# Optimization experiments

Measured on AMD Instinct MI355X. Metric: run time of the kernel, lower is better.

Reference implementation:

```python
import math
import jax, jax.numpy as jnp
import numpy as np

B, S, D, H = 4, 2048, 1024, 16
DK = D // H


def setup_inputs() -> dict:
    key = jax.random.key(0)
    kx, kq, kk, kv, ko = jax.random.split(key, 5)
    scale = 1.0 / math.sqrt(D)
    return {
        "x": jax.random.normal(kx, (B, S, D), dtype=jnp.float32),
        "wq": jax.random.normal(kq, (D, D), dtype=jnp.float32) * scale,
        "wk": jax.random.normal(kk, (D, D), dtype=jnp.float32) * scale,
        "wv": jax.random.normal(kv, (D, D), dtype=jnp.float32) * scale,
        "wo": jax.random.normal(ko, (D, D), dtype=jnp.float32) * scale,
    }


def reference(x, wq, wk, wv, wo):
    b, s, d = x.shape
    # projections -> [b, h, s, dk]
    def split_heads(t):
        return t.reshape(b, s, H, DK).transpose(0, 2, 1, 3)
    q = split_heads(x @ wq)
    k = split_heads(x @ wk)
    v = split_heads(x @ wv)
    # scores [b, h, s, s], scaled by sqrt(d_k)
    scores = jnp.einsum('bhqd,bhkd->bhqk', q, k) / math.sqrt(DK)
    causal = jnp.tril(jnp.ones((s, s), dtype=bool))  # [s, s]
    scores = jnp.where(causal[None, None, :, :], scores, -jnp.inf)
    weights = jax.nn.softmax(scores, axis=-1)
    weights = jnp.nan_to_num(weights, nan=0.0)
    attn = jnp.einsum('bhqk,bhkd->bhqd', weights, v)
    attn = attn.transpose(0, 2, 1, 3).reshape(b, s, d)
    return attn @ wo
```

## Files before the change

### kernel.cpp

```cpp
#include <hip/hip_runtime.h>
#include <hip/hip_bf16.h>
#include <math.h>

#define B_ 4
#define S_ 2048
#define D_ 1024
#define H_ 16
#define DK_ 64

typedef __bf16 bf16;
typedef bf16 bf16x8 __attribute__((ext_vector_type(8)));
typedef float f32x4 __attribute__((ext_vector_type(4)));
typedef float f32x16 __attribute__((ext_vector_type(16)));

__device__ __forceinline__ int swz8(int row, int slot) {
    return row * 64 + ((slot ^ (row & 7)) << 3);
}
__device__ __forceinline__ unsigned packbf(float a, float b) {
    union { bf16 h[2]; unsigned u; } x;
    x.h[0] = (bf16)a; x.h[1] = (bf16)b;
    return x.u;
}
__device__ __forceinline__ void permswap(unsigned& x, unsigned& y) {
    asm("v_permlane32_swap_b32 %0, %1" : "+v"(x), "+v"(y));
}
__device__ __forceinline__ float fexp2(float x) {
#if __has_builtin(__builtin_amdgcn_exp2f)
    return __builtin_amdgcn_exp2f(x);
#else
    float r;
    asm("v_exp_f32 %0, %1" : "=v"(r) : "v"(x));
    return r;
#endif
}
__device__ __forceinline__ void gld16(bf16* lbase, const bf16* gsrc) {
    __builtin_amdgcn_global_load_lds(
        (const __attribute__((address_space(1))) unsigned*)gsrc,
        (__attribute__((address_space(3))) unsigned*)lbase, 16, 0, 0);
}

__global__ __launch_bounds__(256) void prep_kernel(const float* __restrict__ x,
                                                   const float* __restrict__ wq, const float* __restrict__ wk,
                                                   const float* __restrict__ wv, const float* __restrict__ wo,
                                                   bf16* __restrict__ xb, bf16* __restrict__ wqkvT,
                                                   bf16* __restrict__ woT) {
    __shared__ float t[32][33];
    const int bid = blockIdx.x;
    const int tid = threadIdx.x;
    if (bid < 4096) {
        const size_t i = ((size_t)bid * 256 + tid) * 8;
        const float4* src = (const float4*)(x + i);
        float4 f0 = src[0], f1 = src[1];
        bf16x8 v;
        v[0] = (bf16)f0.x; v[1] = (bf16)f0.y; v[2] = (bf16)f0.z; v[3] = (bf16)f0.w;
        v[4] = (bf16)f1.x; v[5] = (bf16)f1.y; v[6] = (bf16)f1.z; v[7] = (bf16)f1.w;
        *(bf16x8*)(xb + i) = v;
    } else {
        const int b2 = bid - 4096;
        const int z = b2 >> 10;
        const float* src = (z == 0) ? wq : (z == 1) ? wk : (z == 2) ? wv : wo;
        bf16* dst = (z < 3) ? (wqkvT + (size_t)z * 1024 * 1024) : woT;
        const int n0 = (b2 & 31) * 32, k0 = ((b2 >> 5) & 31) * 32;
        const int tx = tid & 31, ty = tid >> 5;
#pragma unroll
        for (int j = 0; j < 4; ++j)
            t[ty + j * 8][tx] = src[(size_t)(k0 + ty + j * 8) * 1024 + n0 + tx];
        __syncthreads();
#pragma unroll
        for (int j = 0; j < 4; ++j)
            dst[(size_t)(n0 + ty + j * 8) * 1024 + k0 + tx] = (bf16)t[tx][ty + j * 8];
    }
}

template <int MODE>
__global__ __launch_bounds__(256) void gemm_kernel(const bf16* __restrict__ A, const bf16* __restrict__ Bt,
                                                   void* o0, void* o1, void* o2,
                                                   int M, int N, int K, int NT) {
    __shared__ __align__(16) bf16 As[128 * 64];
    __shared__ __align__(16) bf16 Bs[128 * 64];
    const int tid = threadIdx.x;
    const int lane = tid & 63;
    const int w = tid >> 6;
    const int wm = w >> 1, wn = w & 1;
    const int g = lane >> 4, r16 = lane & 15;

    const int bid = blockIdx.x;
    const int qch = gridDim.x >> 3;
    const int wg = (bid & 7) * qch + (bid >> 3);
    const int mt = wg / NT, nt = wg % NT;
    const int m0 = mt * 128, n0 = nt * 128;

    const int srow = tid >> 3;
    const int sslot = (tid & 7) ^ (srow & 7);
    const bf16* ga = A + (size_t)(m0 + srow) * K + sslot * 8;
    const bf16* gb = Bt + (size_t)(n0 + srow) * K + sslot * 8;

    f32x4 acc[4][4] = {};

    for (int kt = 0; kt < K; kt += 64) {
#pragma unroll
        for (int p = 0; p < 4; ++p) {
            gld16(&As[p * 2048 + w * 512], ga + (size_t)p * 32 * K + kt);
            gld16(&Bs[p * 2048 + w * 512], gb + (size_t)p * 32 * K + kt);
        }
        __syncthreads();
#pragma unroll
        for (int k0 = 0; k0 < 2; ++k0) {
            bf16x8 af[4], bfr[4];
#pragma unroll
            for (int mf = 0; mf < 4; ++mf)
                af[mf] = *(const bf16x8*)&As[swz8(wm * 64 + mf * 16 + r16, 4 * k0 + g)];
#pragma unroll
            for (int nf = 0; nf < 4; ++nf)
                bfr[nf] = *(const bf16x8*)&Bs[swz8(wn * 64 + nf * 16 + r16, 4 * k0 + g)];
#pragma unroll
            for (int mf = 0; mf < 4; ++mf)
#pragma unroll
                for (int nf = 0; nf < 4; ++nf)
                    acc[mf][nf] = __builtin_amdgcn_mfma_f32_16x16x32_bf16(af[mf], bfr[nf], acc[mf][nf], 0, 0, 0);
        }
        __syncthreads();
    }

    if (MODE == 0) {
        const int seg = nt >> 3;
#pragma unroll
        for (int mf = 0; mf < 4; ++mf) {
#pragma unroll
            for (int nf = 0; nf < 4; ++nf) {
                const int col = n0 + wn * 64 + nf * 16 + r16;
                const int n1 = col & 1023;
                const int h = n1 >> 6, dk = n1 & 63;
                const int row0 = m0 + wm * 64 + mf * 16 + 4 * g;
                const int b = row0 >> 11, s0 = row0 & 2047;
                if (seg == 2) {
                    union { bf16 h4[4]; unsigned long long u; } pk;
#pragma unroll
                    for (int rr = 0; rr < 4; ++rr) pk.h4[rr] = (bf16)acc[mf][nf][rr];
                    *(unsigned long long*)((bf16*)o2 + (((size_t)b * H_ + h) * DK_ + dk) * S_ + s0) = pk.u;
                } else {
                    bf16* dst = (seg == 0) ? (bf16*)o0 : (bf16*)o1;
#pragma unroll
                    for (int rr = 0; rr < 4; ++rr)
                        dst[(((size_t)b * H_ + h) * S_ + s0 + rr) * DK_ + dk] = (bf16)acc[mf][nf][rr];
                }
            }
        }
    } else {
#pragma unroll
        for (int mf = 0; mf < 4; ++mf)
#pragma unroll
            for (int nf = 0; nf < 4; ++nf)
#pragma unroll
                for (int rr = 0; rr < 4; ++rr) {
                    int row = m0 + wm * 64 + mf * 16 + 4 * g + rr;
                    int col = n0 + wn * 64 + nf * 16 + r16;
                    ((float*)o0)[(size_t)row * N + col] = acc[mf][nf][rr];
                }
    }
}

__global__ __launch_bounds__(256, 4) void attn_kernel(const bf16* __restrict__ Q,
                                                      const bf16* __restrict__ Kb,
                                                      const bf16* __restrict__ Vt,
                                                      bf16* __restrict__ ctx) {
    __shared__ __align__(16) bf16 lds[4][4096];
    const int bh = blockIdx.x;
    const int qt = 15 - (int)blockIdx.y;
    const int tid = threadIdx.x;
    const int lane = tid & 63, w = tid >> 6;
    const int lq = lane & 31, hi = lane >> 5;
    const int q0 = qt * 128;
    const int q0w = q0 + w * 32;
    const int q = q0w + lq;
    const int njt = 2 * qt + 2;
    const float qscale = 0.125f * 1.44269504088896340736f;

    const int srow = tid >> 3;
    const int sslot = (tid & 7) ^ (srow & 7);
    const bf16* kg = Kb + ((size_t)bh * S_ + srow) * DK_ + sslot * 8;
    const bf16* vg = Vt + ((size_t)bh * DK_ + srow) * S_ + sslot * 8;

    bf16x8 qf[4];
    {
        const bf16* qp = Q + ((size_t)bh * S_ + q) * DK_ + hi * 8;
#pragma unroll
        for (int kc = 0; kc < 4; ++kc) {
            bf16x8 raw = *(const bf16x8*)(qp + kc * 16);
#pragma unroll
            for (int e = 0; e < 8; ++e) qf[kc][e] = (bf16)((float)raw[e] * qscale);
        }
    }

    f32x16 accd[2] = {};
    float lsum = 0.f;

    bf16x8 kreg0 = *(const bf16x8*)kg;
    bf16x8 kreg1 = *(const bf16x8*)(kg + 32 * DK_);
    bf16x8 vreg0 = *(const bf16x8*)vg;
    bf16x8 vreg1 = *(const bf16x8*)(vg + 32 * S_);

    for (int jt = 0; jt < njt; ++jt) {
        const int cur = jt & 1;
        *(bf16x8*)&lds[cur][tid * 8] = kreg0;
        *(bf16x8*)&lds[cur][tid * 8 + 2048] = kreg1;
        *(bf16x8*)&lds[2 + cur][tid * 8] = vreg0;
        *(bf16x8*)&lds[2 + cur][tid * 8 + 2048] = vreg1;
        if (jt + 1 < njt) {
            kreg0 = *(const bf16x8*)(kg + (size_t)(jt + 1) * 64 * DK_);
            kreg1 = *(const bf16x8*)(kg + (size_t)(jt + 1) * 64 * DK_ + 32 * DK_);
            vreg0 = *(const bf16x8*)(vg + (jt + 1) * 64);
            vreg1 = *(const bf16x8*)(vg + (jt + 1) * 64 + 32 * S_);
        }
        __syncthreads();

        if (jt * 64 <= q0w + 31) {
            f32x16 sacc[2];
#pragma unroll
            for (int c = 0; c < 2; ++c)
#pragma unroll
                for (int r = 0; r < 16; ++r) sacc[c][r] = -16.0f;
            __builtin_amdgcn_s_setprio(1);
#pragma unroll
            for (int kc = 0; kc < 4; ++kc) {
#pragma unroll
                for (int c = 0; c < 2; ++c) {
                    bf16x8 kf = *(const bf16x8*)&lds[cur][swz8(c * 32 + lq, kc * 2 + hi)];
                    sacc[c] = __builtin_amdgcn_mfma_f32_32x32x16_bf16(kf, qf[kc], sacc[c], 0, 0, 0);
                }
            }
            __builtin_amdgcn_s_setprio(0);

            if (jt * 64 + 63 > q0w) {
#pragma unroll
                for (int c = 0; c < 2; ++c)
#pragma unroll
                    for (int r = 0; r < 16; ++r) {
                        int key = jt * 64 + c * 32 + (r & 3) + 8 * (r >> 2) + 4 * hi;
                        if (key > q) sacc[c][r] = -INFINITY;
                    }
            }

#pragma unroll
            for (int c = 0; c < 2; ++c)
#pragma unroll
                for (int r = 0; r < 16; ++r) sacc[c][r] = fexp2(sacc[c][r]);

            float s8[8];
#pragma unroll
            for (int i = 0; i < 8; ++i)
                s8[i] = (sacc[0][i] + sacc[0][i + 8]) + (sacc[1][i] + sacc[1][i + 8]);
#pragma unroll
            for (int i = 0; i < 4; ++i) s8[i] += s8[i + 4];
            lsum += (s8[0] + s8[1]) + (s8[2] + s8[3]);

#pragma unroll
            for (int kc = 0; kc < 4; ++kc) {
                const int c = kc >> 1, kf2 = kc & 1;
                unsigned w0 = packbf(sacc[c][8 * kf2 + 0], sacc[c][8 * kf2 + 1]);
                unsigned w1 = packbf(sacc[c][8 * kf2 + 2], sacc[c][8 * kf2 + 3]);
                unsigned w2 = packbf(sacc[c][8 * kf2 + 4], sacc[c][8 * kf2 + 5]);
                unsigned w3 = packbf(sacc[c][8 * kf2 + 6], sacc[c][8 * kf2 + 7]);
                permswap(w0, w2);
                permswap(w1, w3);
                union { unsigned wd[4]; bf16x8 v; } u;
                u.wd[0] = w0; u.wd[1] = w1; u.wd[2] = w2; u.wd[3] = w3;
                __builtin_amdgcn_s_setprio(1);
#pragma unroll
                for (int dt = 0; dt < 2; ++dt) {
                    bf16x8 vf = *(const bf16x8*)&lds[2 + cur][swz8(dt * 32 + lq, kc * 2 + hi)];
                    accd[dt] = __builtin_amdgcn_mfma_f32_32x32x16_bf16(vf, u.v, accd[dt], 0, 0, 0);
                }
                __builtin_amdgcn_s_setprio(0);
            }
        }
    }

    __syncthreads();
    bf16* eb = &lds[0][0];
    const float rl = 1.0f / (lsum + __shfl_xor(lsum, 32));
    {
        const int rowb = (w * 32 + lq) * 128;
        const int rsw = (lq & 7) << 4;
#pragma unroll
        for (int dt = 0; dt < 2; ++dt)
#pragma unroll
            for (int rq = 0; rq < 4; ++rq) {
                union { bf16 h[4]; unsigned long long u64; } pk;
#pragma unroll
                for (int j = 0; j < 4; ++j) pk.h[j] = (bf16)(accd[dt][rq * 4 + j] * rl);
                int off = rowb + ((dt * 64 + rq * 16 + hi * 8) ^ rsw);
                *(unsigned long long*)((char*)eb + off) = pk.u64;
            }
    }
    __syncthreads();
    {
        const int row = tid >> 1, half = tid & 1;
        const int b = bh >> 4, h = bh & 15;
        bf16* op = ctx + ((size_t)b * S_ + q0 + row) * D_ + h * DK_ + half * 32;
#pragma unroll
        for (int i = 0; i < 4; ++i) {
            int sl = half * 4 + i;
            int sls = sl ^ (row & 7);
            bf16x8 v = *(const bf16x8*)((const char*)eb + row * 128 + sls * 16);
            *(bf16x8*)(op + i * 8) = v;
        }
    }
}

extern "C" void kernel_launch(void* const* d_in, const int* in_sizes, int n_in,
                              void* d_out, int out_size, void* d_ws, size_t ws_size,
                              hipStream_t stream) {
    const float* x  = (const float*)d_in[0];
    const float* wq = (const float*)d_in[1];
    const float* wk = (const float*)d_in[2];
    const float* wv = (const float*)d_in[3];
    const float* wo = (const float*)d_in[4];

    char* ws = (char*)d_ws;
    bf16* wqkvT = (bf16*)(ws);
    bf16* woT   = (bf16*)(ws + 6291456);
    bf16* Qb    = (bf16*)(ws + 8388608);
    bf16* Kb    = (bf16*)(ws + 25165824);
    bf16* Vtb   = (bf16*)(ws + 58720256);
    bf16* ctx   = (bf16*)(ws + 75497472);
    bf16* xb    = ctx;

    prep_kernel<<<8192, 256, 0, stream>>>(x, wq, wk, wv, wo, xb, wqkvT, woT);
    gemm_kernel<0><<<1536, 256, 0, stream>>>(xb, wqkvT, Qb, Kb, Vtb, 8192, 3072, 1024, 24);
    attn_kernel<<<dim3(64, 16), 256, 0, stream>>>(Qb, Kb, Vtb, ctx);
    gemm_kernel<1><<<512, 256, 0, stream>>>(ctx, woT, d_out, nullptr, nullptr, 8192, 1024, 1024, 8);
}
```

Measured before the change: 156.3 us.

## Retile QKV projection GEMM to 128x192 tiles with 512-thread blocks

Splits the templated GEMM into a dedicated QKV projection kernel using 128x192 output tiles, 8 waves per block (2x4 wave grid, 64x48 per wave) and 1024 blocks, and a separate output-projection kernel. The larger tile raises arithmetic intensity per LDS load and cuts the block count, which is meant to reduce global and LDS traffic for the QKV GEMM. The cost is a shorter per-wave N extent (3 fragments), more LDS per block, and fewer blocks, which may reduce occupancy or leave tail imbalance across CUs.

New measurement: 145.6 us. 1.07x faster.

```diff
diff --git a/kernel.cpp b/kernel.cpp
--- a/kernel.cpp
+++ b/kernel.cpp
@@ -72,10 +72,83 @@
     }
 }
 
-template <int MODE>
-__global__ __launch_bounds__(256) void gemm_kernel(const bf16* __restrict__ A, const bf16* __restrict__ Bt,
-                                                   void* o0, void* o1, void* o2,
-                                                   int M, int N, int K, int NT) {
+__global__ __launch_bounds__(512) void gemm_qkv_kernel(const bf16* __restrict__ A, const bf16* __restrict__ Bt,
+                                                       bf16* __restrict__ Qb, bf16* __restrict__ Kb,
+                                                       bf16* __restrict__ Vt) {
+    __shared__ __align__(16) bf16 As[128 * 64];
+    __shared__ __align__(16) bf16 Bs[192 * 64];
+    const int tid = threadIdx.x;
+    const int lane = tid & 63;
+    const int w = tid >> 6;
+    const int wm = w >> 2, wn = w & 3;
+    const int g = lane >> 4, r16 = lane & 15;
+
+    const int bid = blockIdx.x;
+    const int wg = (bid & 7) * 128 + (bid >> 3);
+    const int mt = wg >> 4, nt = wg & 15;
+    const int m0 = mt * 128, n0 = nt * 192;
+
+    const int srow = tid >> 3;
+    const int sslot = (tid & 7) ^ (srow & 7);
+    const bf16* ga = A + (size_t)(m0 + srow) * 1024 + sslot * 8;
+    const bf16* gb = Bt + (size_t)(n0 + srow) * 1024 + sslot * 8;
+    const int wbase = w * 512;
+
+    f32x4 acc[4][3] = {};
+
+    for (int kt = 0; kt < 1024; kt += 64) {
+#pragma unroll
+        for (int p = 0; p < 2; ++p)
+            gld16(&As[p * 4096 + wbase], ga + (size_t)p * 64 * 1024 + kt);
+#pragma unroll
+        for (int p = 0; p < 3; ++p)
+            gld16(&Bs[p * 4096 + wbase], gb + (size_t)p * 64 * 1024 + kt);
+        __syncthreads();
+#pragma unroll
+        for (int k0 = 0; k0 < 2; ++k0) {
+            bf16x8 af[4], bfr[3];
+#pragma unroll
+            for (int mf = 0; mf < 4; ++mf)
+                af[mf] = *(const bf16x8*)&As[swz8(wm * 64 + mf * 16 + r16, 4 * k0 + g)];
+#pragma unroll
+            for (int nf = 0; nf < 3; ++nf)
+                bfr[nf] = *(const bf16x8*)&Bs[swz8(wn * 48 + nf * 16 + r16, 4 * k0 + g)];
+#pragma unroll
+            for (int mf = 0; mf < 4; ++mf)
+#pragma unroll
+                for (int nf = 0; nf < 3; ++nf)
+                    acc[mf][nf] = __builtin_amdgcn_mfma_f32_16x16x32_bf16(af[mf], bfr[nf], acc[mf][nf], 0, 0, 0);
+        }
+        __syncthreads();
+    }
+
+#pragma unroll
+    for (int mf = 0; mf < 4; ++mf) {
+#pragma unroll
+        for (int nf = 0; nf < 3; ++nf) {
+            const int col = n0 + wn * 48 + nf * 16 + r16;
+            const int seg = col >> 10;
+            const int n1 = col & 1023;
+            const int h = n1 >> 6, dk = n1 & 63;
+            const int row0 = m0 + wm * 64 + mf * 16 + 4 * g;
+            const int b = row0 >> 11, s0 = row0 & 2047;
+            if (seg == 2) {
+                union { bf16 h4[4]; unsigned long long u; } pk;
+#pragma unroll
+                for (int rr = 0; rr < 4; ++rr) pk.h4[rr] = (bf16)acc[mf][nf][rr];
+                *(unsigned long long*)(Vt + (((size_t)b * H_ + h) * DK_ + dk) * S_ + s0) = pk.u;
+            } else {
+                bf16* dst = (seg == 0) ? Qb : Kb;
+#pragma unroll
+                for (int rr = 0; rr < 4; ++rr)
+                    dst[(((size_t)b * H_ + h) * S_ + s0 + rr) * DK_ + dk] = (bf16)acc[mf][nf][rr];
+            }
+        }
+    }
+}
+
+__global__ __launch_bounds__(256) void gemm_out_kernel(const bf16* __restrict__ A, const bf16* __restrict__ Bt,
+                                                       float* __restrict__ o0, int M, int N, int K, int NT) {
     __shared__ __align__(16) bf16 As[128 * 64];
     __shared__ __align__(16) bf16 Bs[128 * 64];
     const int tid = threadIdx.x;
@@ -122,42 +195,16 @@
         __syncthreads();
     }
 
-    if (MODE == 0) {
-        const int seg = nt >> 3;
-#pragma unroll
-        for (int mf = 0; mf < 4; ++mf) {
-#pragma unroll
-            for (int nf = 0; nf < 4; ++nf) {
-                const int col = n0 + wn * 64 + nf * 16 + r16;
-                const int n1 = col & 1023;
-                const int h = n1 >> 6, dk = n1 & 63;
-                const int row0 = m0 + wm * 64 + mf * 16 + 4 * g;
-                const int b = row0 >> 11, s0 = row0 & 2047;
-                if (seg == 2) {
-                    union { bf16 h4[4]; unsigned long long u; } pk;
-#pragma unroll
-                    for (int rr = 0; rr < 4; ++rr) pk.h4[rr] = (bf16)acc[mf][nf][rr];
-                    *(unsigned long long*)((bf16*)o2 + (((size_t)b * H_ + h) * DK_ + dk) * S_ + s0) = pk.u;
-                } else {
-                    bf16* dst = (seg == 0) ? (bf16*)o0 : (bf16*)o1;
-#pragma unroll
-                    for (int rr = 0; rr < 4; ++rr)
-                        dst[(((size_t)b * H_ + h) * S_ + s0 + rr) * DK_ + dk] = (bf16)acc[mf][nf][rr];
-                }
-            }
-        }
-    } else {
-#pragma unroll
-        for (int mf = 0; mf < 4; ++mf)
-#pragma unroll
-            for (int nf = 0; nf < 4; ++nf)
-#pragma unroll
-                for (int rr = 0; rr < 4; ++rr) {
-                    int row = m0 + wm * 64 + mf * 16 + 4 * g + rr;
-                    int col = n0 + wn * 64 + nf * 16 + r16;
-                    ((float*)o0)[(size_t)row * N + col] = acc[mf][nf][rr];
-                }
-    }
+#pragma unroll
+    for (int mf = 0; mf < 4; ++mf)
+#pragma unroll
+        for (int nf = 0; nf < 4; ++nf)
+#pragma unroll
+            for (int rr = 0; rr < 4; ++rr) {
+                int row = m0 + wm * 64 + mf * 16 + 4 * g + rr;
+                int col = n0 + wn * 64 + nf * 16 + r16;
+                o0[(size_t)row * N + col] = acc[mf][nf][rr];
+            }
 }
 
 __global__ __launch_bounds__(256, 4) void attn_kernel(const bf16* __restrict__ Q,
@@ -327,7 +374,7 @@
     bf16* xb    = ctx;
 
     prep_kernel<<<8192, 256, 0, stream>>>(x, wq, wk, wv, wo, xb, wqkvT, woT);
-    gemm_kernel<0><<<1536, 256, 0, stream>>>(xb, wqkvT, Qb, Kb, Vtb, 8192, 3072, 1024, 24);
+    gemm_qkv_kernel<<<1024, 512, 0, stream>>>(xb, wqkvT, Qb, Kb, Vtb);
     attn_kernel<<<dim3(64, 16), 256, 0, stream>>>(Qb, Kb, Vtb, ctx);
-    gemm_kernel<1><<<512, 256, 0, stream>>>(ctx, woT, d_out, nullptr, nullptr, 8192, 1024, 1024, 8);
-}
+    gemm_out_kernel<<<512, 256, 0, stream>>>(ctx, woT, (float*)d_out, 8192, 1024, 1024, 8);
+}
```
